# Performance work log

Measured on AMD Instinct MI355X. Metric: run time of the kernel, lower is better.

Reference implementation:

```python
import jax, jax.numpy as jnp
import numpy as np

N = 100000      # nodes
E = 1_600_000   # edges
IN = 128        # in_channels
HID = 32        # hidden_channels (per head)
HEADS = 4
NC = 10         # num_classes
NEG_SLOPE = 0.2 # GATConv leaky relu slope
BN_EPS = 1e-5


def _gat_conv(x, src, dst, W, a_src, a_dst, bias, heads, out_ch, concat):
    # x: [N, F_in]; W: [F_in, heads*out_ch]; a_src/a_dst: [heads, out_ch]
    n = x.shape[0]
    h = (x @ W).reshape(n, heads, out_ch)                    # [N,H,C]
    al_src = jnp.sum(h * a_src, axis=-1)                     # [N,H]
    al_dst = jnp.sum(h * a_dst, axis=-1)                     # [N,H]
    e = jax.nn.leaky_relu(al_src[src] + al_dst[dst], NEG_SLOPE)  # [E,H]
    # segment softmax over destination node
    m = jax.ops.segment_max(e, dst, num_segments=n)          # [N,H]
    ex = jnp.exp(e - m[dst])
    s = jax.ops.segment_sum(ex, dst, num_segments=n)         # [N,H]
    alpha = ex / (s[dst] + 1e-16)                            # [E,H]
    out = jax.ops.segment_sum(h[src] * alpha[:, :, None], dst, num_segments=n)  # [N,H,C]
    if concat:
        out = out.reshape(n, heads * out_ch)
    else:
        out = out.mean(axis=1)
    return out + bias


def _bn(x, gamma, beta, mean, var):
    # eval-mode BatchNorm1d with running stats
    return (x - mean) * jax.lax.rsqrt(var + BN_EPS) * gamma + beta


def setup_inputs() -> dict:
    key = jax.random.key(0)
    ks = iter(jax.random.split(key, 40))
    d = {}
    d['x'] = jax.random.normal(next(ks), (N, IN), dtype=jnp.float32)
    d['edge_index'] = jax.random.randint(next(ks), (2, E), 0, N, dtype=jnp.int32)
    dims = [(IN, HID, HEADS), (HID * HEADS, HID, HEADS), (HID * HEADS, HID, 1)]
    for i, (fin, c, h) in enumerate(dims):
        d[f'W{i}'] = jax.random.normal(next(ks), (fin, h * c), dtype=jnp.float32) * (1.0 / np.sqrt(fin))
        d[f'as{i}'] = jax.random.normal(next(ks), (h, c), dtype=jnp.float32) * 0.1
        d[f'ad{i}'] = jax.random.normal(next(ks), (h, c), dtype=jnp.float32) * 0.1
        bdim = h * c if i < 2 else c
        d[f'b{i}'] = jnp.zeros((bdim,), dtype=jnp.float32)
        d[f'g{i}'] = jax.random.uniform(next(ks), (bdim,), dtype=jnp.float32, minval=0.5, maxval=1.5)
        d[f'bt{i}'] = jax.random.normal(next(ks), (bdim,), dtype=jnp.float32) * 0.1
        d[f'm{i}'] = jax.random.normal(next(ks), (bdim,), dtype=jnp.float32) * 0.1
        d[f'v{i}'] = jax.random.uniform(next(ks), (bdim,), dtype=jnp.float32, minval=0.5, maxval=1.5)
    d['Wc'] = jax.random.normal(next(ks), (HID, NC), dtype=jnp.float32) * (1.0 / np.sqrt(HID))
    d['bc'] = jnp.zeros((NC,), dtype=jnp.float32)
    return d


def reference(x, edge_index, W0, as0, ad0, b0, g0, bt0, m0, v0,
              W1, as1, ad1, b1, g1, bt1, m1, v1,
              W2, as2, ad2, b2, g2, bt2, m2, v2, Wc, bc):
    src, dst = edge_index[0], edge_index[1]
    # layer 0: concat heads
    h = _gat_conv(x, src, dst, W0, as0, ad0, b0, HEADS, HID, True)
    h = jax.nn.elu(_bn(h, g0, bt0, m0, v0))
    # layer 1: concat heads
    h = _gat_conv(h, src, dst, W1, as1, ad1, b1, HEADS, HID, True)
    h = jax.nn.elu(_bn(h, g1, bt1, m1, v1))
    # layer 2: single head, no concat
    h = _gat_conv(h, src, dst, W2, as2, ad2, b2, 1, HID, False)
    h = jax.nn.elu(_bn(h, g2, bt2, m2, v2))
    # dropout is identity in eval mode
    return h @ Wc + bc
```

## Files before the change

### kernel.cpp

```cpp
#include <hip/hip_runtime.h>
#include <hip/hip_bf16.h>
#include <math.h>

#define NN   100000
#define NE   1600000
#define FIN  128
#define HID  32
#define NHEADS 4
#define NCLS 10

typedef unsigned int uint32;

__device__ __forceinline__ float bf_lo(uint32 v) {
    return __builtin_bit_cast(float, v << 16);
}
__device__ __forceinline__ float bf_hi(uint32 v) {
    return __builtin_bit_cast(float, v & 0xffff0000u);
}
__device__ __forceinline__ uint32 packbf2(float a, float b) {
    uint32 ua = __builtin_bit_cast(uint32, a);
    uint32 ub = __builtin_bit_cast(uint32, b);
    ua = (ua + 0x7fffu + ((ua >> 16) & 1u)) >> 16;
    ub = (ub + 0x7fffu + ((ub >> 16) & 1u)) & 0xffff0000u;
    return ua | ub;
}

__global__ void zero_i32(int* __restrict__ p, int n) {
    int i = blockIdx.x * blockDim.x + threadIdx.x;
    if (i < n) p[i] = 0;
}

__global__ void hist_rank_kernel(const int* __restrict__ dst, int* __restrict__ cnt,
                                 int* __restrict__ rank, int e) {
    const int t0 = blockIdx.x * (blockDim.x * 4) + threadIdx.x;
    int d[4];
    bool a[4];
#pragma unroll
    for (int k = 0; k < 4; ++k) {
        const int j = t0 + k * 256;
        a[k] = (j < e);
        d[k] = a[k] ? dst[j] : 0;
    }
    int r[4];
#pragma unroll
    for (int k = 0; k < 4; ++k)
        if (a[k]) r[k] = atomicAdd(&cnt[d[k]], 1);
#pragma unroll
    for (int k = 0; k < 4; ++k) {
        const int j = t0 + k * 256;
        if (a[k]) rank[j] = r[k];
    }
}

__global__ void scan_block_sums(const int* __restrict__ cnt, int* __restrict__ bsum, int n) {
    __shared__ int sm[256];
    int i = blockIdx.x * 256 + threadIdx.x;
    int v = (i < n) ? cnt[i] : 0;
    sm[threadIdx.x] = v;
    __syncthreads();
    for (int off = 128; off > 0; off >>= 1) {
        if (threadIdx.x < off) sm[threadIdx.x] += sm[threadIdx.x + off];
        __syncthreads();
    }
    if (threadIdx.x == 0) bsum[blockIdx.x] = sm[0];
}

__global__ void scan_single(const int* __restrict__ bsum, int* __restrict__ boff, int nb) {
    __shared__ int sm[512];
    int t = threadIdx.x;
    int v = (t < nb) ? bsum[t] : 0;
    sm[t] = v;
    __syncthreads();
    for (int off = 1; off < 512; off <<= 1) {
        int u = (t >= off) ? sm[t - off] : 0;
        __syncthreads();
        sm[t] += u;
        __syncthreads();
    }
    if (t < nb) boff[t] = sm[t] - v;
}

__global__ void scan_final(const int* __restrict__ cnt, const int* __restrict__ boff,
                           int* __restrict__ rowptr, int n) {
    __shared__ int sm[256];
    int i = blockIdx.x * 256 + threadIdx.x;
    int v = (i < n) ? cnt[i] : 0;
    sm[threadIdx.x] = v;
    __syncthreads();
    for (int off = 1; off < 256; off <<= 1) {
        int u = (threadIdx.x >= off) ? sm[threadIdx.x - off] : 0;
        __syncthreads();
        sm[threadIdx.x] += u;
        __syncthreads();
    }
    int incl = sm[threadIdx.x];
    int excl = incl - v;
    if (i < n) rowptr[i] = boff[blockIdx.x] + excl;
    if (i == n - 1) rowptr[n] = boff[blockIdx.x] + incl;
}

__global__ void scatter_kernel(const int* __restrict__ src, const int* __restrict__ dst,
                               const int* __restrict__ rank, const int* __restrict__ rowptr,
                               int* __restrict__ esrc, int e) {
    const int t0 = blockIdx.x * (blockDim.x * 4) + threadIdx.x;
#pragma unroll
    for (int k = 0; k < 4; ++k) {
        const int j = t0 + k * 256;
        if (j < e) {
            const int d = dst[j];
            esrc[rowptr[d] + rank[j]] = src[j];
        }
    }
}

template <int FOUT, int H>
__global__ __launch_bounds__(256) void gemm_tiled(const float* __restrict__ X,
                                                  const float* __restrict__ Wm,
                                                  const float* __restrict__ a_s,
                                                  const float* __restrict__ a_d,
                                                  float* __restrict__ alS,
                                                  float* __restrict__ alD,
                                                  uint32* __restrict__ Outb, int n) {
    constexpr int K   = 128;
    constexpr int KC  = 32;
    constexpr int MT  = 128;
    constexpr int CPT = FOUT / 16;
    constexpr int C   = FOUT / H;
    constexpr int TPH = 16 / H;
    __shared__ float As[KC][MT + 1];
    __shared__ float Bs[KC][FOUT];

    const int t   = threadIdx.x;
    const int tx  = t & 15;
    const int ty  = t >> 4;
    const int row0 = blockIdx.x * MT;

    float acc[8][CPT];
#pragma unroll
    for (int i = 0; i < 8; ++i)
#pragma unroll
        for (int j = 0; j < CPT; ++j) acc[i][j] = 0.f;

    for (int kc = 0; kc < K; kc += KC) {
#pragma unroll
        for (int i = 0; i < 4; ++i) {
            const int l  = t + i * 256;
            const int ar = l >> 3;
            const int af = l & 7;
            int grow = row0 + ar;
            if (grow >= n) grow = n - 1;
            const float4 v = *(const float4*)(X + (size_t)grow * K + kc + af * 4);
            As[af * 4 + 0][ar] = v.x;
            As[af * 4 + 1][ar] = v.y;
            As[af * 4 + 2][ar] = v.z;
            As[af * 4 + 3][ar] = v.w;
        }
        constexpr int BF4 = KC * FOUT / 4;
#pragma unroll
        for (int i = 0; i < BF4 / 256; ++i) {
            const int l   = t + i * 256;
            const int br  = l / (FOUT / 4);
            const int bc4 = l % (FOUT / 4);
            const float4 v = *(const float4*)(Wm + (size_t)(kc + br) * FOUT + bc4 * 4);
            *(float4*)&Bs[br][bc4 * 4] = v;
        }
        __syncthreads();

#pragma unroll 8
        for (int k = 0; k < KC; ++k) {
            float a[8], b[CPT];
#pragma unroll
            for (int i = 0; i < 8; ++i) a[i] = As[k][ty * 8 + i];
#pragma unroll
            for (int j = 0; j < CPT; ++j) b[j] = Bs[k][tx * CPT + j];
#pragma unroll
            for (int i = 0; i < 8; ++i)
#pragma unroll
                for (int j = 0; j < CPT; ++j)
                    acc[i][j] = fmaf(a[i], b[j], acc[i][j]);
        }
        __syncthreads();
    }

    const int h     = tx / TPH;
    const int cbase = (tx % TPH) * CPT;
    float av[CPT], dv[CPT];
#pragma unroll
    for (int j = 0; j < CPT; ++j) {
        av[j] = a_s[h * C + cbase + j];
        dv[j] = a_d[h * C + cbase + j];
    }

#pragma unroll
    for (int i = 0; i < 8; ++i) {
        const int grow = row0 + ty * 8 + i;
        if (grow < n) {
            uint32* bp = Outb + ((size_t)grow * FOUT + tx * CPT) / 2;
            if constexpr (CPT == 8) {
                uint4 pb;
                pb.x = packbf2(acc[i][0], acc[i][1]);
                pb.y = packbf2(acc[i][2], acc[i][3]);
                pb.z = packbf2(acc[i][4], acc[i][5]);
                pb.w = packbf2(acc[i][6], acc[i][7]);
                *(uint4*)bp = pb;
            } else {
                *bp = packbf2(acc[i][0], acc[i][1]);
            }
        }
        float ps = 0.f, pd = 0.f;
#pragma unroll
        for (int j = 0; j < CPT; ++j) {
            ps = fmaf(acc[i][j], av[j], ps);
            pd = fmaf(acc[i][j], dv[j], pd);
        }
#pragma unroll
        for (int off = 1; off < TPH; off <<= 1) {
            ps += __shfl_xor(ps, off);
            pd += __shfl_xor(pd, off);
        }
        if ((tx % TPH) == 0 && grow < n) {
            alS[(size_t)grow * H + h] = ps;
            alD[(size_t)grow * H + h] = pd;
        }
    }
}

template <int H, int C>
__global__ __launch_bounds__(256) void gat_aggregate(
    const uint32* __restrict__ Hb,
    const int* __restrict__ rowptr, const int* __restrict__ esrc,
    const float* __restrict__ alS, const float* __restrict__ alD,
    const float* __restrict__ bias, const float* __restrict__ gamma,
    const float* __restrict__ beta, const float* __restrict__ bnmean,
    const float* __restrict__ bnvar, float* __restrict__ Out, int n) {
    constexpr int F  = H * C;
    constexpr int RW = F / 2;
    constexpr int NW = 4;
    __shared__ __align__(16) int   s_src[NW][68];
    __shared__ __align__(16) float s_ex[NW][H][68];

    const int wave = threadIdx.x >> 6;
    const int lane = threadIdx.x & 63;
    const int d    = blockIdx.x * NW + wave;
    if (d >= n) return;

    if (lane < 4) {
        s_src[wave][64 + lane] = 0;
#pragma unroll
        for (int h = 0; h < H; ++h) s_ex[wave][h][64 + lane] = 0.f;
    }
    __builtin_amdgcn_wave_barrier();

    const int beg = rowptr[d], end = rowptr[d + 1];
    float al_d[H], sl[H];
#pragma unroll
    for (int h = 0; h < H; ++h) {
        al_d[h] = alD[(size_t)d * H + h];
        sl[h]   = 0.f;
    }
    float acc0 = 0.f, acc1 = 0.f;
    const int head = (H == 4) ? (lane >> 4) : 0;

    for (int base = beg; base < end; base += 64) {
        const int j   = base + lane;
        const bool act = (j < end);
        int sj = 0;
        float ex[H];
        if (act) {
            sj = esrc[j];
            if constexpr (H == 4) {
                float4 av = *(const float4*)(alS + (size_t)sj * 4);
                float t0 = av.x + al_d[0], t1 = av.y + al_d[1];
                float t2 = av.z + al_d[2], t3 = av.w + al_d[3];
                t0 = t0 > 0.f ? t0 : 0.2f * t0;
                t1 = t1 > 0.f ? t1 : 0.2f * t1;
                t2 = t2 > 0.f ? t2 : 0.2f * t2;
                t3 = t3 > 0.f ? t3 : 0.2f * t3;
                ex[0] = __expf(t0); ex[1] = __expf(t1);
                ex[2] = __expf(t2); ex[3] = __expf(t3);
            } else {
                float t0 = alS[sj] + al_d[0];
                t0 = t0 > 0.f ? t0 : 0.2f * t0;
                ex[0] = __expf(t0);
            }
        } else {
#pragma unroll
            for (int h = 0; h < H; ++h) ex[h] = 0.f;
        }
#pragma unroll
        for (int h = 0; h < H; ++h) {
            s_ex[wave][h][lane] = ex[h];
            sl[h] += ex[h];
        }
        s_src[wave][lane] = sj;
        __builtin_amdgcn_wave_barrier();

        const int cc = min(64, end - base);
        if constexpr (H == 4) {
            for (int jj = 0; jj < cc; jj += 4) {
                const int4   s4 = *(const int4*)&s_src[wave][jj];
                const float4 w4 = *(const float4*)&s_ex[wave][head][jj];
                const int b0 = __builtin_amdgcn_readfirstlane(s4.x);
                const int b1 = __builtin_amdgcn_readfirstlane(s4.y);
                const int b2 = __builtin_amdgcn_readfirstlane(s4.z);
                const int b3 = __builtin_amdgcn_readfirstlane(s4.w);
                const uint32 v0 = Hb[(size_t)b0 * RW + lane];
                const uint32 v1 = Hb[(size_t)b1 * RW + lane];
                const uint32 v2 = Hb[(size_t)b2 * RW + lane];
                const uint32 v3 = Hb[(size_t)b3 * RW + lane];
                acc0 = fmaf(bf_lo(v0), w4.x, acc0); acc1 = fmaf(bf_hi(v0), w4.x, acc1);
                acc0 = fmaf(bf_lo(v1), w4.y, acc0); acc1 = fmaf(bf_hi(v1), w4.y, acc1);
                acc0 = fmaf(bf_lo(v2), w4.z, acc0); acc1 = fmaf(bf_hi(v2), w4.z, acc1);
                acc0 = fmaf(bf_lo(v3), w4.w, acc0); acc1 = fmaf(bf_hi(v3), w4.w, acc1);
            }
        } else {
            const int g  = lane >> 4;
            const int li = lane & 15;
            for (int jj = 0; jj < cc; jj += 4) {
                const int   idx = jj + g;
                const int   sj2 = s_src[wave][idx];
                const float w   = s_ex[wave][0][idx];
                const uint32 v  = Hb[(size_t)sj2 * RW + li];
                acc0 = fmaf(bf_lo(v), w, acc0);
                acc1 = fmaf(bf_hi(v), w, acc1);
            }
        }
        __builtin_amdgcn_wave_barrier();
    }

#pragma unroll
    for (int h = 0; h < H; ++h) {
#pragma unroll
        for (int off = 32; off > 0; off >>= 1) sl[h] += __shfl_xor(sl[h], off);
    }
    float sh;
    if constexpr (H == 4) {
        float a = (head & 1) ? sl[1] : sl[0];
        float b = (head & 1) ? sl[3] : sl[2];
        sh = (head & 2) ? b : a;
    } else {
        sh = sl[0];
        acc0 += __shfl_xor(acc0, 16); acc0 += __shfl_xor(acc0, 32);
        acc1 += __shfl_xor(acc1, 16); acc1 += __shfl_xor(acc1, 32);
    }

    const float inv = 1.f / (sh + 1e-16f);
    const int li  = (F == 128) ? lane : (lane & 15);
    const int c0 = 2 * li, c1 = 2 * li + 1;
    const bool wr = (F == 128) || (lane < 16);
    if (wr) {
        float o0 = acc0 * inv, o1 = acc1 * inv;
        float y0 = (o0 + bias[c0] - bnmean[c0]) * rsqrtf(bnvar[c0] + 1e-5f) * gamma[c0] + beta[c0];
        float y1 = (o1 + bias[c1] - bnmean[c1]) * rsqrtf(bnvar[c1] + 1e-5f) * gamma[c1] + beta[c1];
        y0 = y0 > 0.f ? y0 : expm1f(y0);
        y1 = y1 > 0.f ? y1 : expm1f(y1);
        *(float2*)(Out + (size_t)d * F + c0) = make_float2(y0, y1);
    }
}

__global__ void classifier_kernel(const float* __restrict__ H3, const float* __restrict__ Wc,
                                  const float* __restrict__ bc, float* __restrict__ out, int n) {
    int t  = blockIdx.x * blockDim.x + threadIdx.x;
    int ni = t / NCLS, c = t % NCLS;
    if (ni >= n) return;
    const float* row = H3 + (size_t)ni * HID;
    float a = bc[c];
#pragma unroll
    for (int k = 0; k < HID; ++k) a = fmaf(row[k], Wc[k * NCLS + c], a);
    out[(size_t)ni * NCLS + c] = a;
}

static inline char* align256(char* p) {
    return (char*)(((uintptr_t)p + 255) & ~(uintptr_t)255);
}

extern "C" void kernel_launch(void* const* d_in, const int* in_sizes, int n_in,
                              void* d_out, int out_size, void* d_ws, size_t ws_size,
                              hipStream_t stream) {
    const float* x  = (const float*)d_in[0];
    const int*   ei = (const int*)d_in[1];
    const int N = in_sizes[0] / FIN;
    const int E = in_sizes[1] / 2;
    const int* src = ei;
    const int* dst = ei + E;

    const float *W0 = (const float*)d_in[2],  *as0 = (const float*)d_in[3],
                *ad0 = (const float*)d_in[4], *b0 = (const float*)d_in[5],
                *g0 = (const float*)d_in[6],  *bt0 = (const float*)d_in[7],
                *m0 = (const float*)d_in[8],  *v0 = (const float*)d_in[9];
    const float *W1 = (const float*)d_in[10], *as1 = (const float*)d_in[11],
                *ad1 = (const float*)d_in[12],*b1 = (const float*)d_in[13],
                *g1 = (const float*)d_in[14], *bt1 = (const float*)d_in[15],
                *m1 = (const float*)d_in[16], *v1 = (const float*)d_in[17];
    const float *W2 = (const float*)d_in[18], *as2 = (const float*)d_in[19],
                *ad2 = (const float*)d_in[20],*b2 = (const float*)d_in[21],
                *g2 = (const float*)d_in[22], *bt2 = (const float*)d_in[23],
                *m2 = (const float*)d_in[24], *v2 = (const float*)d_in[25];
    const float *Wc = (const float*)d_in[26], *bc = (const float*)d_in[27];
    float* out = (float*)d_out;

    char* p = (char*)d_ws;
    uint32* Abf = (uint32*)p;   p = align256(p + (size_t)N * FIN * 2);
    float* B = (float*)p;       p = align256(p + (size_t)N * FIN * 4);
    float* alS = (float*)p;     p = align256(p + (size_t)N * NHEADS * 4);
    float* alD = (float*)p;     p = align256(p + (size_t)N * NHEADS * 4);
    int* cnt = (int*)p;         p = align256(p + (size_t)N * 4);
    int* rowptr = (int*)p;      p = align256(p + (size_t)(N + 1) * 4);
    int* rank = (int*)p;        p = align256(p + (size_t)E * 4);
    int* esrc = (int*)p;        p = align256(p + (size_t)E * 4);
    int* bsum = (int*)p;        p = align256(p + 512 * 4);
    int* boff = (int*)p;        p = align256(p + 512 * 4);
    (void)ws_size; (void)n_in; (void)out_size;

    const int NB = (N + 255) / 256;
    const int EB4 = (E + 1023) / 1024;

    zero_i32<<<NB, 256, 0, stream>>>(cnt, N);
    hist_rank_kernel<<<EB4, 256, 0, stream>>>(dst, cnt, rank, E);
    scan_block_sums<<<NB, 256, 0, stream>>>(cnt, bsum, N);
    scan_single<<<1, 512, 0, stream>>>(bsum, boff, NB);
    scan_final<<<NB, 256, 0, stream>>>(cnt, boff, rowptr, N);
    scatter_kernel<<<EB4, 256, 0, stream>>>(src, dst, rank, rowptr, esrc, E);

    const int GB = (N + 127) / 128;

    gemm_tiled<128, 4><<<GB, 256, 0, stream>>>(x, W0, as0, ad0, alS, alD, Abf, N);
    gat_aggregate<4, 32><<<(N + 3) / 4, 256, 0, stream>>>(Abf, rowptr, esrc, alS, alD,
                                                          b0, g0, bt0, m0, v0, B, N);
    gemm_tiled<128, 4><<<GB, 256, 0, stream>>>(B, W1, as1, ad1, alS, alD, Abf, N);
    gat_aggregate<4, 32><<<(N + 3) / 4, 256, 0, stream>>>(Abf, rowptr, esrc, alS, alD,
                                                          b1, g1, bt1, m1, v1, B, N);
    gemm_tiled<32, 1><<<GB, 256, 0, stream>>>(B, W2, as2, ad2, alS, alD, Abf, N);
    gat_aggregate<1, 32><<<(N + 3) / 4, 256, 0, stream>>>(Abf, rowptr, esrc, alS, alD,
                                                          b2, g2, bt2, m2, v2, B, N);
    classifier_kernel<<<(N * NCLS + 255) / 256, 256, 0, stream>>>(B, Wc, bc, out, N);
}
```

Before: 603.0 us.

## Pack multiple destination nodes per wave with 16-byte gathers in GAT aggregation

The aggregation kernel now assigns a group of lanes to each destination node: 16 lanes for 128 features, 4 lanes for 32. A wave therefore handles 4 or 16 nodes at once, and each lane gathers 8 bf16 features with a single 16-byte load. This targets poor lane utilisation when the average degree is about 16 rather than 64, and cuts the number of load instructions. The GEMM also switches to vectorized float4 shared-memory reads and pads As rows to 132 floats. In exchange, divergence grows, since a wave loops until its highest-degree node is finished.

```diff
diff --git a/kernel.cpp b/kernel.cpp
--- a/kernel.cpp
+++ b/kernel.cpp
@@ -23,6 +23,17 @@
     ua = (ua + 0x7fffu + ((ua >> 16) & 1u)) >> 16;
     ub = (ub + 0x7fffu + ((ub >> 16) & 1u)) & 0xffff0000u;
     return ua | ub;
+}
+
+__device__ __forceinline__ void fma8(float* acc, uint4 v, float w) {
+    acc[0] = fmaf(bf_lo(v.x), w, acc[0]);
+    acc[1] = fmaf(bf_hi(v.x), w, acc[1]);
+    acc[2] = fmaf(bf_lo(v.y), w, acc[2]);
+    acc[3] = fmaf(bf_hi(v.y), w, acc[3]);
+    acc[4] = fmaf(bf_lo(v.z), w, acc[4]);
+    acc[5] = fmaf(bf_hi(v.z), w, acc[5]);
+    acc[6] = fmaf(bf_lo(v.w), w, acc[6]);
+    acc[7] = fmaf(bf_hi(v.w), w, acc[7]);
 }
 
 __global__ void zero_i32(int* __restrict__ p, int n) {
@@ -127,8 +138,8 @@
     constexpr int CPT = FOUT / 16;
     constexpr int C   = FOUT / H;
     constexpr int TPH = 16 / H;
-    __shared__ float As[KC][MT + 1];
-    __shared__ float Bs[KC][FOUT];
+    __shared__ __align__(16) float As[KC][132];
+    __shared__ __align__(16) float Bs[KC][FOUT];
 
     const int t   = threadIdx.x;
     const int tx  = t & 15;
@@ -168,11 +179,19 @@
 
 #pragma unroll 8
         for (int k = 0; k < KC; ++k) {
-            float a[8], b[CPT];
-#pragma unroll
-            for (int i = 0; i < 8; ++i) a[i] = As[k][ty * 8 + i];
-#pragma unroll
-            for (int j = 0; j < CPT; ++j) b[j] = Bs[k][tx * CPT + j];
+            const float4 a0 = *(const float4*)&As[k][ty * 8];
+            const float4 a1 = *(const float4*)&As[k][ty * 8 + 4];
+            const float a[8] = {a0.x, a0.y, a0.z, a0.w, a1.x, a1.y, a1.z, a1.w};
+            float b[CPT];
+            if constexpr (CPT == 8) {
+                const float4 b0 = *(const float4*)&Bs[k][tx * 8];
+                const float4 b1 = *(const float4*)&Bs[k][tx * 8 + 4];
+                b[0] = b0.x; b[1] = b0.y; b[2] = b0.z; b[3] = b0.w;
+                b[4] = b1.x; b[5] = b1.y; b[6] = b1.z; b[7] = b1.w;
+            } else {
+                const float2 b0 = *(const float2*)&Bs[k][tx * 2];
+                b[0] = b0.x; b[1] = b0.y;
+            }
 #pragma unroll
             for (int i = 0; i < 8; ++i)
 #pragma unroll
@@ -233,128 +252,133 @@
     const float* __restrict__ bias, const float* __restrict__ gamma,
     const float* __restrict__ beta, const float* __restrict__ bnmean,
     const float* __restrict__ bnvar, float* __restrict__ Out, int n) {
-    constexpr int F  = H * C;
-    constexpr int RW = F / 2;
-    constexpr int NW = 4;
+    constexpr int F   = H * C;
+    constexpr int RW  = F / 2;
+    constexpr int GL  = F / 8;
+    constexpr int GPW = 64 / GL;
+    constexpr int NW  = 4;
+    constexpr int DPB = NW * GPW;
+    __shared__ __align__(16) float s_ex[NW][H][68];
     __shared__ __align__(16) int   s_src[NW][68];
-    __shared__ __align__(16) float s_ex[NW][H][68];
 
     const int wave = threadIdx.x >> 6;
     const int lane = threadIdx.x & 63;
-    const int d    = blockIdx.x * NW + wave;
-    if (d >= n) return;
-
-    if (lane < 4) {
-        s_src[wave][64 + lane] = 0;
-#pragma unroll
-        for (int h = 0; h < H; ++h) s_ex[wave][h][64 + lane] = 0.f;
-    }
-    __builtin_amdgcn_wave_barrier();
-
-    const int beg = rowptr[d], end = rowptr[d + 1];
-    float al_d[H], sl[H];
-#pragma unroll
-    for (int h = 0; h < H; ++h) {
-        al_d[h] = alD[(size_t)d * H + h];
-        sl[h]   = 0.f;
-    }
-    float acc0 = 0.f, acc1 = 0.f;
-    const int head = (H == 4) ? (lane >> 4) : 0;
-
-    for (int base = beg; base < end; base += 64) {
-        const int j   = base + lane;
-        const bool act = (j < end);
-        int sj = 0;
-        float ex[H];
-        if (act) {
-            sj = esrc[j];
+    const int g    = lane / GL;
+    const int li   = lane % GL;
+    const int hsel = (H == 4) ? (li >> 2) : 0;
+    const int d    = blockIdx.x * DPB + wave * GPW + g;
+
+    int beg = 0, end = 0;
+    if (d < n) { beg = rowptr[d]; end = rowptr[d + 1]; }
+    const int deg = end - beg;
+
+    float al_d[H];
+#pragma unroll
+    for (int h = 0; h < H; ++h) al_d[h] = 0.f;
+    if (d < n) {
+        if constexpr (H == 4) {
+            const float4 v = *(const float4*)(alD + (size_t)d * 4);
+            al_d[0] = v.x; al_d[1] = v.y; al_d[2] = v.z; al_d[3] = v.w;
+        } else {
+            al_d[0] = alD[d];
+        }
+    }
+
+    float sl[H];
+#pragma unroll
+    for (int h = 0; h < H; ++h) sl[h] = 0.f;
+    float acc[8];
+#pragma unroll
+    for (int j = 0; j < 8; ++j) acc[j] = 0.f;
+
+    for (int it = 0;; ++it) {
+        const int rem = deg - it * GL;
+        int mr = rem;
+#pragma unroll
+        for (int off = GL; off < 64; off <<= 1)
+            mr = max(mr, __shfl_xor(mr, off));
+        if (mr <= 0) break;
+
+        if (li < rem) {
+            const int sj = esrc[beg + it * GL + li];
+            s_src[wave][lane] = sj;
             if constexpr (H == 4) {
-                float4 av = *(const float4*)(alS + (size_t)sj * 4);
+                const float4 av = *(const float4*)(alS + (size_t)sj * 4);
                 float t0 = av.x + al_d[0], t1 = av.y + al_d[1];
                 float t2 = av.z + al_d[2], t3 = av.w + al_d[3];
                 t0 = t0 > 0.f ? t0 : 0.2f * t0;
                 t1 = t1 > 0.f ? t1 : 0.2f * t1;
                 t2 = t2 > 0.f ? t2 : 0.2f * t2;
                 t3 = t3 > 0.f ? t3 : 0.2f * t3;
-                ex[0] = __expf(t0); ex[1] = __expf(t1);
-                ex[2] = __expf(t2); ex[3] = __expf(t3);
+                const float e0 = __expf(t0), e1 = __expf(t1);
+                const float e2 = __expf(t2), e3 = __expf(t3);
+                s_ex[wave][0][lane] = e0; s_ex[wave][1][lane] = e1;
+                s_ex[wave][2][lane] = e2; s_ex[wave][3][lane] = e3;
+                sl[0] += e0; sl[1] += e1; sl[2] += e2; sl[3] += e3;
             } else {
                 float t0 = alS[sj] + al_d[0];
                 t0 = t0 > 0.f ? t0 : 0.2f * t0;
-                ex[0] = __expf(t0);
+                const float e0 = __expf(t0);
+                s_ex[wave][0][lane] = e0;
+                sl[0] += e0;
             }
-        } else {
-#pragma unroll
-            for (int h = 0; h < H; ++h) ex[h] = 0.f;
-        }
-#pragma unroll
-        for (int h = 0; h < H; ++h) {
-            s_ex[wave][h][lane] = ex[h];
-            sl[h] += ex[h];
-        }
-        s_src[wave][lane] = sj;
+        }
         __builtin_amdgcn_wave_barrier();
 
-        const int cc = min(64, end - base);
-        if constexpr (H == 4) {
-            for (int jj = 0; jj < cc; jj += 4) {
-                const int4   s4 = *(const int4*)&s_src[wave][jj];
-                const float4 w4 = *(const float4*)&s_ex[wave][head][jj];
-                const int b0 = __builtin_amdgcn_readfirstlane(s4.x);
-                const int b1 = __builtin_amdgcn_readfirstlane(s4.y);
-                const int b2 = __builtin_amdgcn_readfirstlane(s4.z);
-                const int b3 = __builtin_amdgcn_readfirstlane(s4.w);
-                const uint32 v0 = Hb[(size_t)b0 * RW + lane];
-                const uint32 v1 = Hb[(size_t)b1 * RW + lane];
-                const uint32 v2 = Hb[(size_t)b2 * RW + lane];
-                const uint32 v3 = Hb[(size_t)b3 * RW + lane];
-                acc0 = fmaf(bf_lo(v0), w4.x, acc0); acc1 = fmaf(bf_hi(v0), w4.x, acc1);
-                acc0 = fmaf(bf_lo(v1), w4.y, acc0); acc1 = fmaf(bf_hi(v1), w4.y, acc1);
-                acc0 = fmaf(bf_lo(v2), w4.z, acc0); acc1 = fmaf(bf_hi(v2), w4.z, acc1);
-                acc0 = fmaf(bf_lo(v3), w4.w, acc0); acc1 = fmaf(bf_hi(v3), w4.w, acc1);
+        const int cc = min(GL, mr);
+        for (int e0 = 0; e0 < cc; e0 += 4) {
+            const int rr = rem - e0;
+            if (rr > 0) {
+                const int4   s4 = *(const int4*)  &s_src[wave][g * GL + e0];
+                const float4 w4 = *(const float4*)&s_ex[wave][hsel][g * GL + e0];
+                if (rr >= 4) {
+                    const uint4 v0 = *(const uint4*)(Hb + (size_t)s4.x * RW + li * 4);
+                    const uint4 v1 = *(const uint4*)(Hb + (size_t)s4.y * RW + li * 4);
+                    const uint4 v2 = *(const uint4*)(Hb + (size_t)s4.z * RW + li * 4);
+                    const uint4 v3 = *(const uint4*)(Hb + (size_t)s4.w * RW + li * 4);
+                    fma8(acc, v0, w4.x);
+                    fma8(acc, v1, w4.y);
+                    fma8(acc, v2, w4.z);
+                    fma8(acc, v3, w4.w);
+                } else {
+                    {
+                        const uint4 v = *(const uint4*)(Hb + (size_t)s4.x * RW + li * 4);
+                        fma8(acc, v, w4.x);
+                    }
+                    if (rr > 1) {
+                        const uint4 v = *(const uint4*)(Hb + (size_t)s4.y * RW + li * 4);
+                        fma8(acc, v, w4.y);
+                    }
+                    if (rr > 2) {
+                        const uint4 v = *(const uint4*)(Hb + (size_t)s4.z * RW + li * 4);
+                        fma8(acc, v, w4.z);
+                    }
+                }
             }
-        } else {
-            const int g  = lane >> 4;
-            const int li = lane & 15;
-            for (int jj = 0; jj < cc; jj += 4) {
-                const int   idx = jj + g;
-                const int   sj2 = s_src[wave][idx];
-                const float w   = s_ex[wave][0][idx];
-                const uint32 v  = Hb[(size_t)sj2 * RW + li];
-                acc0 = fmaf(bf_lo(v), w, acc0);
-                acc1 = fmaf(bf_hi(v), w, acc1);
-            }
         }
         __builtin_amdgcn_wave_barrier();
     }
 
 #pragma unroll
-    for (int h = 0; h < H; ++h) {
-#pragma unroll
-        for (int off = 32; off > 0; off >>= 1) sl[h] += __shfl_xor(sl[h], off);
-    }
-    float sh;
-    if constexpr (H == 4) {
-        float a = (head & 1) ? sl[1] : sl[0];
-        float b = (head & 1) ? sl[3] : sl[2];
-        sh = (head & 2) ? b : a;
-    } else {
-        sh = sl[0];
-        acc0 += __shfl_xor(acc0, 16); acc0 += __shfl_xor(acc0, 32);
-        acc1 += __shfl_xor(acc1, 16); acc1 += __shfl_xor(acc1, 32);
-    }
-
-    const float inv = 1.f / (sh + 1e-16f);
-    const int li  = (F == 128) ? lane : (lane & 15);
-    const int c0 = 2 * li, c1 = 2 * li + 1;
-    const bool wr = (F == 128) || (lane < 16);
-    if (wr) {
-        float o0 = acc0 * inv, o1 = acc1 * inv;
-        float y0 = (o0 + bias[c0] - bnmean[c0]) * rsqrtf(bnvar[c0] + 1e-5f) * gamma[c0] + beta[c0];
-        float y1 = (o1 + bias[c1] - bnmean[c1]) * rsqrtf(bnvar[c1] + 1e-5f) * gamma[c1] + beta[c1];
-        y0 = y0 > 0.f ? y0 : expm1f(y0);
-        y1 = y1 > 0.f ? y1 : expm1f(y1);
-        *(float2*)(Out + (size_t)d * F + c0) = make_float2(y0, y1);
+    for (int h = 0; h < H; ++h)
+#pragma unroll
+        for (int off = 1; off < GL; off <<= 1)
+            sl[h] += __shfl_xor(sl[h], off);
+
+    const float inv = 1.f / (sl[hsel] + 1e-16f);
+    if (d < n) {
+        const int c0 = li * 8;
+        float y[8];
+#pragma unroll
+        for (int jj = 0; jj < 8; ++jj) {
+            const int c = c0 + jj;
+            const float o = acc[jj] * inv;
+            float yy = (o + bias[c] - bnmean[c]) * rsqrtf(bnvar[c] + 1e-5f) * gamma[c] + beta[c];
+            y[jj] = yy > 0.f ? yy : expm1f(yy);
+        }
+        float* op = Out + (size_t)d * F + c0;
+        *(float4*)(op)     = make_float4(y[0], y[1], y[2], y[3]);
+        *(float4*)(op + 4) = make_float4(y[4], y[5], y[6], y[7]);
     }
 }
 
@@ -425,13 +449,13 @@
     const int GB = (N + 127) / 128;
 
     gemm_tiled<128, 4><<<GB, 256, 0, stream>>>(x, W0, as0, ad0, alS, alD, Abf, N);
-    gat_aggregate<4, 32><<<(N + 3) / 4, 256, 0, stream>>>(Abf, rowptr, esrc, alS, alD,
-                                                          b0, g0, bt0, m0, v0, B, N);
+    gat_aggregate<4, 32><<<(N + 15) / 16, 256, 0, stream>>>(Abf, rowptr, esrc, alS, alD,
+                                                            b0, g0, bt0, m0, v0, B, N);
     gemm_tiled<128, 4><<<GB, 256, 0, stream>>>(B, W1, as1, ad1, alS, alD, Abf, N);
-    gat_aggregate<4, 32><<<(N + 3) / 4, 256, 0, stream>>>(Abf, rowptr, esrc, alS, alD,
-                                                          b1, g1, bt1, m1, v1, B, N);
+    gat_aggregate<4, 32><<<(N + 15) / 16, 256, 0, stream>>>(Abf, rowptr, esrc, alS, alD,
+                                                            b1, g1, bt1, m1, v1, B, N);
     gemm_tiled<32, 1><<<GB, 256, 0, stream>>>(B, W2, as2, ad2, alS, alD, Abf, N);
-    gat_aggregate<1, 32><<<(N + 3) / 4, 256, 0, stream>>>(Abf, rowptr, esrc, alS, alD,
-                                                          b2, g2, bt2, m2, v2, B, N);
+    gat_aggregate<1, 32><<<(N + 63) / 64, 256, 0, stream>>>(Abf, rowptr, esrc, alS, alD,
+                                                            b2, g2, bt2, m2, v2, B, N);
     classifier_kernel<<<(N * NCLS + 255) / 256, 256, 0, stream>>>(B, Wc, bc, out, N);
 }
```

New measurement: 745.0 us. +23.6%, slower.
